# Performance work log

Measured on AMD Instinct MI355X. Metric: run time of the kernel, lower is better.

## Reference

```python
import jax, jax.numpy as jnp
import numpy as np

TRIM = 0.2
EPS = 1e-06
BIG = 1e30  # sentinel pushing invalid pixels to the end of the sort


def setup_inputs() -> dict:
    key = jax.random.key(0)
    k1, k2, k3 = jax.random.split(key, 3)
    B, C, H, W = 32, 1, 384, 1280
    pred = jax.random.normal(k1, (B, C, H, W), dtype=jnp.float32)
    gt = jax.random.normal(k2, (B, C, H, W), dtype=jnp.float32)
    mask = jax.random.randint(k3, (B, C, H, W), 0, 2, dtype=jnp.int32)
    return {"pred": pred, "gt": gt, "mask": mask}


def _per_sample_loss(p, g, m):
    # p, g: [N] float; m: [N] bool
    mf = m.astype(p.dtype)
    n = mf.sum()                      # number of valid pixels (float)
    n_safe = jnp.maximum(n, 1.0)
    # masked least-squares scale/shift: alpha = cov(d,z)/var(d), beta = mean_z - alpha*mean_d
    mean_d = jnp.sum(p * mf) / n_safe
    mean_z = jnp.sum(g * mf) / n_safe
    var_d = jnp.sum(p * p * mf) / n_safe - mean_d * mean_d
    cov_dz = jnp.sum(p * g * mf) / n_safe - mean_d * mean_z
    alpha = cov_dz / (var_d + EPS)
    beta = mean_z - alpha * mean_d
    # residuals; invalid pixels pushed to the tail of the sort
    res = jnp.abs(alpha * p + beta - g)
    res = jnp.where(m, res, BIG)
    res_sorted = jnp.sort(res)
    # keep the k = floor((1-trim)*n) smallest residuals
    k = jnp.floor((1.0 - TRIM) * n).astype(jnp.int32)
    keep = jnp.arange(res.shape[0], dtype=jnp.int32) < k
    kept_sum = jnp.sum(jnp.where(keep, res_sorted, 0.0))
    mean_kept = kept_sum / jnp.maximum(k.astype(p.dtype), 1.0)
    return jnp.where(k > 0, mean_kept, 0.0)


def reference(pred, gt, mask):
    B = pred.shape[0]
    p = pred.reshape(B, -1)
    g = gt.reshape(B, -1)
    m = mask.reshape(B, -1) > 0
    per_b = jax.vmap(_per_sample_loss)(p, g, m)  # [B]
    return jnp.mean(per_b)
```

## Files before the change

### kernel.cpp

```cpp
#include <hip/hip_runtime.h>
#include <hip/hip_fp16.h>
#include <stdint.h>

#define NB 32
#define NPIX 491520
#define NT 256

#define K1CHUNKS 60
#define K1CHUNK 8192
#define K1HALF4 (K1CHUNK / 8)

#define K2CHUNKS 32
#define K2CHUNK 15360
#define K2IT (K2CHUNK / 4 / NT)

#define NBINS 4096

#define CNT1 (1ull << 40)
#define SLOWMASK ((1ull << 40) - 1ull)

typedef float  vf4 __attribute__((ext_vector_type(4)));
typedef int    vi4 __attribute__((ext_vector_type(4)));

struct Ws {
  double moments[NB][5];
  double losses[NB];
  unsigned long long hist64[NB][NBINS];
};

__device__ __forceinline__ double wave_sum_d(double v) {
#pragma unroll
  for (int o = 32; o > 0; o >>= 1) v += __shfl_down(v, o, 64);
  return v;
}

__device__ __forceinline__ double block_sum_d(double v, double* red4) {
  v = wave_sum_d(v);
  const int lane = threadIdx.x & 63, w = threadIdx.x >> 6;
  if (lane == 0) red4[w] = v;
  __syncthreads();
  return red4[0] + red4[1] + red4[2] + red4[3];
}

__device__ __forceinline__ int k_from_n(double n) {
  return (int)floorf(0.8f * (float)n);
}

__device__ __forceinline__ void coef_from_moments(const Ws* ws, int b, float* a_out, float* be_out) {
  const double n = ws->moments[b][0];
  const double ns = n > 1.0 ? n : 1.0;
  const double md = ws->moments[b][1] / ns;
  const double mz = ws->moments[b][2] / ns;
  const double var = ws->moments[b][3] / ns - md * md;
  const double cov = ws->moments[b][4] / ns - md * mz;
  const double a = cov / (var + 1e-6);
  *a_out = (float)a;
  *be_out = (float)(mz - a * md);
}

__device__ __forceinline__ double bin_sum(int bin, unsigned long long h) {
  const double cnt = (double)(h >> 40);
  const double slow = (double)(h & SLOWMASK);
  const int e = bin >> 4, t4 = bin & 15;
  if (e == 0)
    return ldexp(cnt * (double)(t4 << 19) + slow, -149);
  return ldexp(cnt * (1.0 + (double)t4 * 0.0625) + slow * (1.0 / 8388608.0), e - 127);
}

template <bool PACK>
__global__ __launch_bounds__(NT, 8) void k_mom(
    const float* __restrict__ pred, const float* __restrict__ gt,
    const int* __restrict__ mask, Ws* __restrict__ ws,
    uint32_t* __restrict__ packed) {
  const int b = blockIdx.y;
  const size_t base = (size_t)b * NPIX + (size_t)blockIdx.x * K1CHUNK;
  const vf4* p4 = (const vf4*)(pred + base);
  const vf4* g4 = (const vf4*)(gt + base);
  const vi4* m4 = (const vi4*)(mask + base);
  uint4* o4 = (uint4*)(packed + base);
  float n = 0.f, sp = 0.f, sg = 0.f, spp = 0.f, spg = 0.f;
  for (int i = threadIdx.x; i < K1HALF4; i += NT) {
    vf4 pa = __builtin_nontemporal_load(&p4[i]);
    vf4 pb = __builtin_nontemporal_load(&p4[i + K1HALF4]);
    vf4 ga = __builtin_nontemporal_load(&g4[i]);
    vf4 gb = __builtin_nontemporal_load(&g4[i + K1HALF4]);
    vi4 ma = __builtin_nontemporal_load(&m4[i]);
    vi4 mb = __builtin_nontemporal_load(&m4[i + K1HALF4]);
    const float pe[8] = {pa.x, pa.y, pa.z, pa.w, pb.x, pb.y, pb.z, pb.w};
    const float ge[8] = {ga.x, ga.y, ga.z, ga.w, gb.x, gb.y, gb.z, gb.w};
    const int   me[8] = {ma.x, ma.y, ma.z, ma.w, mb.x, mb.y, mb.z, mb.w};
    uint32_t pk[8];
#pragma unroll
    for (int j = 0; j < 8; j++) {
      const float mf = me[j] ? 1.f : 0.f;
      const float pm = pe[j] * mf;
      const float gm = ge[j] * mf;
      n += mf; sp += pm; sg += gm;
      spp = fmaf(pe[j], pm, spp);
      spg = fmaf(pe[j], gm, spg);
      if (PACK) {
        const uint32_t hp = (uint32_t)__half_as_ushort(__float2half_rn(pe[j]));
        const uint32_t hg = (uint32_t)__half_as_ushort(__float2half_rn(ge[j]));
        pk[j] = me[j] ? (hp | (hg << 16)) : (hp | 0x7C000000u);
      }
    }
    if (PACK) {
      uint4 oa; oa.x = pk[0]; oa.y = pk[1]; oa.z = pk[2]; oa.w = pk[3];
      uint4 ob; ob.x = pk[4]; ob.y = pk[5]; ob.z = pk[6]; ob.w = pk[7];
      o4[i] = oa;
      o4[i + K1HALF4] = ob;
    }
  }
  __shared__ double red4[4];
  double v[5] = {(double)n, (double)sp, (double)sg, (double)spp, (double)spg};
#pragma unroll
  for (int q = 0; q < 5; q++) {
    const double s = block_sum_d(v[q], red4);
    if (threadIdx.x == 0) atomicAdd(&ws->moments[b][q], s);
    __syncthreads();
  }
  const int flat = (b * K1CHUNKS + (int)blockIdx.x) * NT + (int)threadIdx.x;
  if (flat < NB * NBINS) ((unsigned long long*)ws->hist64)[flat] = 0ull;
}

template <bool PACKED>
__global__ __launch_bounds__(NT, 4) void k_hist(
    const uint32_t* __restrict__ packed,
    const float* __restrict__ pred, const float* __restrict__ gt,
    const int* __restrict__ mask, Ws* __restrict__ ws) {
  __shared__ unsigned long long h64[NBINS];
  for (int i = threadIdx.x; i < NBINS; i += NT) h64[i] = 0ull;
  const int b = blockIdx.y;
  float a, be;
  coef_from_moments(ws, b, &a, &be);
  __syncthreads();
  const size_t base = (size_t)b * NPIX + (size_t)blockIdx.x * K2CHUNK;
  if (PACKED) {
    const uint4* u4 = (const uint4*)(packed + base);
    for (int j = 0; j < K2IT; j++) {
      const uint4 u = u4[j * NT + threadIdx.x];
      const uint32_t ue[4] = {u.x, u.y, u.z, u.w};
#pragma unroll
      for (int l = 0; l < 4; l++) {
        const uint32_t uu = ue[l];
        if ((uu >> 16) == 0x7C00u) continue;
        const __half2 h2 = __builtin_bit_cast(__half2, uu);
        const float r = fabsf(fmaf(a, __low2float(h2), be) - __high2float(h2));
        const uint32_t t = __float_as_uint(r);
        atomicAdd(&h64[t >> 19], CNT1 | (unsigned long long)(t & 0x7FFFFu));
      }
    }
  } else {
    const float4* p4 = (const float4*)(pred + base);
    const float4* g4 = (const float4*)(gt + base);
    const int4*   m4 = (const int4*)(mask + base);
    for (int j = 0; j < K2IT; j++) {
      const int i = j * NT + (int)threadIdx.x;
      float4 p = p4[i]; float4 g = g4[i]; int4 m = m4[i];
      const float pe[4] = {p.x, p.y, p.z, p.w};
      const float ge[4] = {g.x, g.y, g.z, g.w};
      const int   me[4] = {m.x, m.y, m.z, m.w};
#pragma unroll
      for (int l = 0; l < 4; l++) {
        if (!me[l]) continue;
        const float r = fabsf(fmaf(a, pe[l], be) - ge[l]);
        const uint32_t t = __float_as_uint(r);
        atomicAdd(&h64[t >> 19], CNT1 | (unsigned long long)(t & 0x7FFFFu));
      }
    }
  }
  __syncthreads();
  for (int i = threadIdx.x; i < NBINS; i += NT) {
    const unsigned long long v = h64[i];
    if (v) atomicAdd(&ws->hist64[b][i], v);
  }
}

__global__ __launch_bounds__(NT) void k_fin(Ws* __restrict__ ws) {
  const int b = (int)blockIdx.x;
  const int tid = (int)threadIdx.x;
  __shared__ int pc[NT];
  __shared__ int shX, shCum;
  __shared__ double red4[4];
  const unsigned long long* H = ws->hist64[b];
  unsigned long long h[16];
  int lc = 0;
#pragma unroll
  for (int j = 0; j < 16; j++) { h[j] = H[tid * 16 + j]; lc += (int)(h[j] >> 40); }
  pc[tid] = lc;
  if (tid == 0) { shX = NBINS; shCum = 0; }
  __syncthreads();
  int pre = 0;
  for (int t = 0; t < tid; t++) pre += pc[t];
  const int k = k_from_n(ws->moments[b][0]);
  if (k > 0 && pre < k && pre + lc >= k) {
    int cum = pre;
#pragma unroll
    for (int j = 0; j < 16; j++) {
      const int c = (int)(h[j] >> 40);
      if (cum + c >= k) { shX = tid * 16 + j; shCum = cum; break; }
      cum += c;
    }
  }
  __syncthreads();
  const int X = shX;
  double below = 0.0;
#pragma unroll
  for (int j = 0; j < 16; j++) {
    const int idx = tid * 16 + j;
    if (idx < X) below += bin_sum(idx, h[j]);
  }
  const double tot = block_sum_d(below, red4);
  if (tid == 0) {
    double loss = 0.0;
    if (k > 0 && X < NBINS) {
      const unsigned long long hX = H[X];
      const double cX = (double)(hX >> 40);
      const double partial = (double)(k - shCum) * (bin_sum(X, hX) / cX);
      loss = (tot + partial) / (double)k;
    }
    ws->losses[b] = loss;
  }
}

__global__ void k_out(const Ws* __restrict__ ws, float* __restrict__ out) {
  double v = (threadIdx.x < NB) ? ws->losses[threadIdx.x] : 0.0;
  v = wave_sum_d(v);
  if (threadIdx.x == 0) out[0] = (float)(v / (double)NB);
}

extern "C" void kernel_launch(void* const* d_in, const int* in_sizes, int n_in,
                              void* d_out, int out_size, void* d_ws, size_t ws_size,
                              hipStream_t stream) {
  const float* pred = (const float*)d_in[0];
  const float* gt   = (const float*)d_in[1];
  const int*   mask = (const int*)d_in[2];
  float* out = (float*)d_out;
  Ws* ws = (Ws*)d_ws;

  const size_t poff = (sizeof(Ws) + 255) & ~(size_t)255;
  const size_t pbytes = (size_t)NB * NPIX * sizeof(uint32_t);
  const bool packed_ok = ws_size >= poff + pbytes;
  uint32_t* packed = (uint32_t*)((char*)d_ws + poff);

  (void)hipMemsetAsync(d_ws, 0, sizeof(double) * NB * 6, stream);

  dim3 g1(K1CHUNKS, NB);
  dim3 g2(K2CHUNKS, NB);
  if (packed_ok) {
    k_mom<true><<<g1, NT, 0, stream>>>(pred, gt, mask, ws, packed);
    k_hist<true><<<g2, NT, 0, stream>>>(packed, pred, gt, mask, ws);
  } else {
    k_mom<false><<<g1, NT, 0, stream>>>(pred, gt, mask, ws, nullptr);
    k_hist<false><<<g2, NT, 0, stream>>>(nullptr, pred, gt, mask, ws);
  }
  k_fin<<<NB, NT, 0, stream>>>(ws);
  k_out<<<1, 64, 0, stream>>>(ws, out);
}
```

Before: 209.0 us.

## Replace fp16 packed intermediate with a 1-bit mask bitmap and re-read fp32 inputs

The first pass no longer writes a 4-byte-per-pixel fp16 pack of pred and gt. It now writes a 1-bit-per-pixel validity bitmap, built through shared-memory nibbles. The histogram pass re-reads pred and gt in fp32 with nontemporal loads and takes the mask from the bitmap staged in shared memory. This removes the large intermediate write and the fp16 rounding of residuals, but pass two now reads 8 bytes per pixel from the original inputs instead of 4, so total traffic stays about the same.

```diff
diff --git a/kernel.cpp b/kernel.cpp
--- a/kernel.cpp
+++ b/kernel.cpp
@@ -1,5 +1,4 @@
 #include <hip/hip_runtime.h>
-#include <hip/hip_fp16.h>
 #include <stdint.h>
 
 #define NB 32
@@ -9,10 +8,13 @@
 #define K1CHUNKS 60
 #define K1CHUNK 8192
 #define K1HALF4 (K1CHUNK / 8)
+#define K1GROUPS (K1CHUNK / 4)
+#define K1WORDS (K1CHUNK / 64)
 
 #define K2CHUNKS 32
 #define K2CHUNK 15360
 #define K2IT (K2CHUNK / 4 / NT)
+#define K2WORDS (K2CHUNK / 64)
 
 #define NBINS 4096
 
@@ -67,17 +69,18 @@
   return ldexp(cnt * (1.0 + (double)t4 * 0.0625) + slow * (1.0 / 8388608.0), e - 127);
 }
 
-template <bool PACK>
+template <bool BM>
 __global__ __launch_bounds__(NT, 8) void k_mom(
     const float* __restrict__ pred, const float* __restrict__ gt,
     const int* __restrict__ mask, Ws* __restrict__ ws,
-    uint32_t* __restrict__ packed) {
+    unsigned long long* __restrict__ bm) {
   const int b = blockIdx.y;
   const size_t base = (size_t)b * NPIX + (size_t)blockIdx.x * K1CHUNK;
   const vf4* p4 = (const vf4*)(pred + base);
   const vf4* g4 = (const vf4*)(gt + base);
   const vi4* m4 = (const vi4*)(mask + base);
-  uint4* o4 = (uint4*)(packed + base);
+  __shared__ unsigned char nib[K1GROUPS];
+  __shared__ double red4[4];
   float n = 0.f, sp = 0.f, sg = 0.f, spp = 0.f, spg = 0.f;
   for (int i = threadIdx.x; i < K1HALF4; i += NT) {
     vf4 pa = __builtin_nontemporal_load(&p4[i]);
@@ -89,7 +92,6 @@
     const float pe[8] = {pa.x, pa.y, pa.z, pa.w, pb.x, pb.y, pb.z, pb.w};
     const float ge[8] = {ga.x, ga.y, ga.z, ga.w, gb.x, gb.y, gb.z, gb.w};
     const int   me[8] = {ma.x, ma.y, ma.z, ma.w, mb.x, mb.y, mb.z, mb.w};
-    uint32_t pk[8];
 #pragma unroll
     for (int j = 0; j < 8; j++) {
       const float mf = me[j] ? 1.f : 0.f;
@@ -98,20 +100,25 @@
       n += mf; sp += pm; sg += gm;
       spp = fmaf(pe[j], pm, spp);
       spg = fmaf(pe[j], gm, spg);
-      if (PACK) {
-        const uint32_t hp = (uint32_t)__half_as_ushort(__float2half_rn(pe[j]));
-        const uint32_t hg = (uint32_t)__half_as_ushort(__float2half_rn(ge[j]));
-        pk[j] = me[j] ? (hp | (hg << 16)) : (hp | 0x7C000000u);
-      }
-    }
-    if (PACK) {
-      uint4 oa; oa.x = pk[0]; oa.y = pk[1]; oa.z = pk[2]; oa.w = pk[3];
-      uint4 ob; ob.x = pk[4]; ob.y = pk[5]; ob.z = pk[6]; ob.w = pk[7];
-      o4[i] = oa;
-      o4[i + K1HALF4] = ob;
-    }
-  }
-  __shared__ double red4[4];
+    }
+    if (BM) {
+      nib[i] = (unsigned char)((me[0] ? 1 : 0) | (me[1] ? 2 : 0) |
+                               (me[2] ? 4 : 0) | (me[3] ? 8 : 0));
+      nib[i + K1HALF4] = (unsigned char)((me[4] ? 1 : 0) | (me[5] ? 2 : 0) |
+                                         (me[6] ? 4 : 0) | (me[7] ? 8 : 0));
+    }
+  }
+  if (BM) {
+    __syncthreads();
+    if (threadIdx.x < K1WORDS) {
+      unsigned long long w = 0;
+#pragma unroll
+      for (int j = 0; j < 16; j++)
+        w |= (unsigned long long)nib[threadIdx.x * 16 + j] << (4 * j);
+      bm[base / 64 + threadIdx.x] = w;
+    }
+    __syncthreads();
+  }
   double v[5] = {(double)n, (double)sp, (double)sg, (double)spp, (double)spg};
 #pragma unroll
   for (int q = 0; q < 5; q++) {
@@ -123,50 +130,46 @@
   if (flat < NB * NBINS) ((unsigned long long*)ws->hist64)[flat] = 0ull;
 }
 
-template <bool PACKED>
+template <bool BM>
 __global__ __launch_bounds__(NT, 4) void k_hist(
-    const uint32_t* __restrict__ packed,
     const float* __restrict__ pred, const float* __restrict__ gt,
-    const int* __restrict__ mask, Ws* __restrict__ ws) {
+    const int* __restrict__ mask, const unsigned long long* __restrict__ bm,
+    Ws* __restrict__ ws) {
   __shared__ unsigned long long h64[NBINS];
+  __shared__ unsigned long long smask[K2WORDS];
   for (int i = threadIdx.x; i < NBINS; i += NT) h64[i] = 0ull;
   const int b = blockIdx.y;
+  const size_t base = (size_t)b * NPIX + (size_t)blockIdx.x * K2CHUNK;
+  if (BM) {
+    if (threadIdx.x < K2WORDS) smask[threadIdx.x] = bm[base / 64 + threadIdx.x];
+  }
   float a, be;
   coef_from_moments(ws, b, &a, &be);
   __syncthreads();
-  const size_t base = (size_t)b * NPIX + (size_t)blockIdx.x * K2CHUNK;
-  if (PACKED) {
-    const uint4* u4 = (const uint4*)(packed + base);
-    for (int j = 0; j < K2IT; j++) {
-      const uint4 u = u4[j * NT + threadIdx.x];
-      const uint32_t ue[4] = {u.x, u.y, u.z, u.w};
-#pragma unroll
-      for (int l = 0; l < 4; l++) {
-        const uint32_t uu = ue[l];
-        if ((uu >> 16) == 0x7C00u) continue;
-        const __half2 h2 = __builtin_bit_cast(__half2, uu);
-        const float r = fabsf(fmaf(a, __low2float(h2), be) - __high2float(h2));
-        const uint32_t t = __float_as_uint(r);
-        atomicAdd(&h64[t >> 19], CNT1 | (unsigned long long)(t & 0x7FFFFu));
-      }
-    }
-  } else {
-    const float4* p4 = (const float4*)(pred + base);
-    const float4* g4 = (const float4*)(gt + base);
-    const int4*   m4 = (const int4*)(mask + base);
-    for (int j = 0; j < K2IT; j++) {
-      const int i = j * NT + (int)threadIdx.x;
-      float4 p = p4[i]; float4 g = g4[i]; int4 m = m4[i];
-      const float pe[4] = {p.x, p.y, p.z, p.w};
-      const float ge[4] = {g.x, g.y, g.z, g.w};
-      const int   me[4] = {m.x, m.y, m.z, m.w};
-#pragma unroll
-      for (int l = 0; l < 4; l++) {
-        if (!me[l]) continue;
-        const float r = fabsf(fmaf(a, pe[l], be) - ge[l]);
-        const uint32_t t = __float_as_uint(r);
-        atomicAdd(&h64[t >> 19], CNT1 | (unsigned long long)(t & 0x7FFFFu));
-      }
+  const vf4* p4 = (const vf4*)(pred + base);
+  const vf4* g4 = (const vf4*)(gt + base);
+  const vi4* m4 = (const vi4*)(mask + base);
+  for (int j = 0; j < K2IT; j++) {
+    const int i = j * NT + (int)threadIdx.x;
+    const vf4 p = __builtin_nontemporal_load(&p4[i]);
+    const vf4 g = __builtin_nontemporal_load(&g4[i]);
+    const float pe[4] = {p.x, p.y, p.z, p.w};
+    const float ge[4] = {g.x, g.y, g.z, g.w};
+    int me[4];
+    if (BM) {
+      const unsigned int nb4 =
+          (unsigned int)(smask[i >> 4] >> ((i & 15) * 4)) & 0xFu;
+      me[0] = nb4 & 1; me[1] = nb4 & 2; me[2] = nb4 & 4; me[3] = nb4 & 8;
+    } else {
+      const vi4 m = __builtin_nontemporal_load(&m4[i]);
+      me[0] = m.x; me[1] = m.y; me[2] = m.z; me[3] = m.w;
+    }
+#pragma unroll
+    for (int l = 0; l < 4; l++) {
+      if (!me[l]) continue;
+      const float r = fabsf(fmaf(a, pe[l], be) - ge[l]);
+      const uint32_t t = __float_as_uint(r);
+      atomicAdd(&h64[t >> 19], CNT1 | (unsigned long long)(t & 0x7FFFFu));
     }
   }
   __syncthreads();
@@ -238,21 +241,21 @@
   float* out = (float*)d_out;
   Ws* ws = (Ws*)d_ws;
 
-  const size_t poff = (sizeof(Ws) + 255) & ~(size_t)255;
-  const size_t pbytes = (size_t)NB * NPIX * sizeof(uint32_t);
-  const bool packed_ok = ws_size >= poff + pbytes;
-  uint32_t* packed = (uint32_t*)((char*)d_ws + poff);
+  const size_t boff = (sizeof(Ws) + 255) & ~(size_t)255;
+  const size_t bbytes = (size_t)NB * NPIX / 8;
+  const bool bm_ok = ws_size >= boff + bbytes;
+  unsigned long long* bm = (unsigned long long*)((char*)d_ws + boff);
 
   (void)hipMemsetAsync(d_ws, 0, sizeof(double) * NB * 6, stream);
 
   dim3 g1(K1CHUNKS, NB);
   dim3 g2(K2CHUNKS, NB);
-  if (packed_ok) {
-    k_mom<true><<<g1, NT, 0, stream>>>(pred, gt, mask, ws, packed);
-    k_hist<true><<<g2, NT, 0, stream>>>(packed, pred, gt, mask, ws);
+  if (bm_ok) {
+    k_mom<true><<<g1, NT, 0, stream>>>(pred, gt, mask, ws, bm);
+    k_hist<true><<<g2, NT, 0, stream>>>(pred, gt, mask, bm, ws);
   } else {
     k_mom<false><<<g1, NT, 0, stream>>>(pred, gt, mask, ws, nullptr);
-    k_hist<false><<<g2, NT, 0, stream>>>(nullptr, pred, gt, mask, ws);
+    k_hist<false><<<g2, NT, 0, stream>>>(pred, gt, mask, nullptr, ws);
   }
   k_fin<<<NB, NT, 0, stream>>>(ws);
   k_out<<<1, 64, 0, stream>>>(ws, out);
```

Result: no change. 208.8 us (-0.1%).
